# Performance work log

Measured on AMD Instinct MI355X. Metric: run time of the kernel, lower is better.

The kernel has to match this reference:

```python
import jax, jax.numpy as jnp
import numpy as np

NUM_NODES = 50000
NUM_EDGES = 1250000
FEAT_DIM = 64

def setup_inputs() -> dict:
    key = jax.random.key(0)
    k1, k2 = jax.random.split(key)
    msg = jax.random.normal(k1, (NUM_EDGES, FEAT_DIM), dtype=jnp.float32)
    edge_index = jax.random.randint(k2, (2, NUM_EDGES), 0, NUM_NODES, dtype=jnp.int64)
    return {"msg": msg, "edge_index": edge_index}

def reference(msg, edge_index):
    # Original: one_hot(edge_index[1], num_nodes).T @ msg  ==  segment-sum over dst nodes.
    # We compute the same math without materializing the [N, E] one-hot matrix.
    dst = edge_index[1]
    h = jax.ops.segment_sum(msg, dst, num_segments=NUM_NODES)  # [num_nodes, feat_dim]
    return h
```

## Files before the change

kernel.cpp:

```cpp
#include <hip/hip_runtime.h>
#include <hip/hip_bf16.h>

#define NUM_NODES 50000
#define NUM_EDGES 1250000
#define FEAT_DIM  64

#define CAP 80

#define WS_COUNTS   0
#define WS_EDGEIDS  50048

typedef float vfloat4 __attribute__((ext_vector_type(4)));

__global__ void scatter_slots_kernel(const int4* __restrict__ dst4,
                                     int* __restrict__ counts,
                                     int* __restrict__ edge_ids) {
    int t = blockIdx.x * blockDim.x + threadIdx.x;
    if (t < NUM_EDGES / 4) {
        int4 d = dst4[t];
        int e = t * 4;
        int s0 = atomicAdd(&counts[d.x], 1);
        int s1 = atomicAdd(&counts[d.y], 1);
        int s2 = atomicAdd(&counts[d.z], 1);
        int s3 = atomicAdd(&counts[d.w], 1);
        edge_ids[d.x * CAP + s0] = e;
        edge_ids[d.y * CAP + s1] = e + 1;
        edge_ids[d.z * CAP + s2] = e + 2;
        edge_ids[d.w * CAP + s3] = e + 3;
    }
}

__global__ __launch_bounds__(256) void gather_kernel(
    const vfloat4* __restrict__ msg4,
    const int* __restrict__ counts,
    const int* __restrict__ edge_ids,
    vfloat4* __restrict__ out4)
{
    int node  = blockIdx.x * 16 + (threadIdx.x >> 4);
    int chunk = threadIdx.x & 15;
    int cnt = counts[node];
    cnt = (cnt > CAP) ? CAP : cnt;
    const int* ids = edge_ids + node * CAP;
    vfloat4 a0 = 0.f, a1 = 0.f, a2 = 0.f, a3 = 0.f;
    int j = 0;
    for (; j + 3 < cnt; j += 4) {
        int e0 = ids[j];
        int e1 = ids[j + 1];
        int e2 = ids[j + 2];
        int e3 = ids[j + 3];
        a0 += __builtin_nontemporal_load(&msg4[(size_t)e0 * 16 + chunk]);
        a1 += __builtin_nontemporal_load(&msg4[(size_t)e1 * 16 + chunk]);
        a2 += __builtin_nontemporal_load(&msg4[(size_t)e2 * 16 + chunk]);
        a3 += __builtin_nontemporal_load(&msg4[(size_t)e3 * 16 + chunk]);
    }
    for (; j < cnt; j++) {
        int e0 = ids[j];
        a0 += __builtin_nontemporal_load(&msg4[(size_t)e0 * 16 + chunk]);
    }
    out4[(size_t)node * 16 + chunk] = (a0 + a1) + (a2 + a3);
}

extern "C" void kernel_launch(void* const* d_in, const int* in_sizes, int n_in,
                              void* d_out, int out_size, void* d_ws, size_t ws_size,
                              hipStream_t stream) {
    const float* msg = (const float*)d_in[0];
    const int* edge_index = (const int*)d_in[1];
    const int* dst = edge_index + NUM_EDGES;
    float* out = (float*)d_out;

    int* ws       = (int*)d_ws;
    int* counts   = ws + WS_COUNTS;
    int* edge_ids = ws + WS_EDGEIDS;

    hipMemsetAsync(counts, 0, 50048 * sizeof(int), stream);

    scatter_slots_kernel<<<(NUM_EDGES / 4 + 255) / 256, 256, 0, stream>>>(
        (const int4*)dst, counts, edge_ids);

    gather_kernel<<<NUM_NODES / 16, 256, 0, stream>>>(
        (const vfloat4*)msg, counts, edge_ids, (vfloat4*)out);
}
```

Baseline: 495.3 us.

## Assign one wavefront per node with shuffled edge ids and cross-slot reduction

The gather kernel now gives each node a full 64-lane wavefront instead of 16 lanes. Edge ids are loaded cooperatively, one per lane, and broadcast with shuffles. Four slots of 16 lanes each handle a different edge, and the partial sums are combined with xor shuffles before one slot writes the output. This is meant to spread the work better across nodes with varying degree, expose more memory parallelism per node and remove the dependent per-thread id loads. The cost is four times as many blocks, plus shuffle and reduction overhead.

```diff
diff --git a/kernel.cpp b/kernel.cpp
--- a/kernel.cpp
+++ b/kernel.cpp
@@ -36,28 +36,37 @@
     const int* __restrict__ edge_ids,
     vfloat4* __restrict__ out4)
 {
-    int node  = blockIdx.x * 16 + (threadIdx.x >> 4);
-    int chunk = threadIdx.x & 15;
+    int node = blockIdx.x * 4 + (threadIdx.x >> 6);
+    int lane = threadIdx.x & 63;
     int cnt = counts[node];
     cnt = (cnt > CAP) ? CAP : cnt;
     const int* ids = edge_ids + node * CAP;
-    vfloat4 a0 = 0.f, a1 = 0.f, a2 = 0.f, a3 = 0.f;
-    int j = 0;
-    for (; j + 3 < cnt; j += 4) {
-        int e0 = ids[j];
-        int e1 = ids[j + 1];
-        int e2 = ids[j + 2];
-        int e3 = ids[j + 3];
-        a0 += __builtin_nontemporal_load(&msg4[(size_t)e0 * 16 + chunk]);
-        a1 += __builtin_nontemporal_load(&msg4[(size_t)e1 * 16 + chunk]);
-        a2 += __builtin_nontemporal_load(&msg4[(size_t)e2 * 16 + chunk]);
-        a3 += __builtin_nontemporal_load(&msg4[(size_t)e3 * 16 + chunk]);
+    int chunk = lane & 15;
+    int slot  = lane >> 4;
+    vfloat4 acc0 = 0.f, acc1 = 0.f;
+    for (int base = 0; base < cnt; base += 64) {
+        int n = cnt - base;
+        n = (n > 64) ? 64 : n;
+        int eid = (lane < n) ? ids[base + lane] : -1;
+        int T = (n + 3) >> 2;
+        int i = 0;
+        for (; i + 1 < T; i += 2) {
+            int e0 = __shfl(eid, 4 * i + slot);
+            int e1 = __shfl(eid, 4 * i + 4 + slot);
+            if (e0 >= 0) acc0 += __builtin_nontemporal_load(&msg4[(size_t)e0 * 16 + chunk]);
+            if (e1 >= 0) acc1 += __builtin_nontemporal_load(&msg4[(size_t)e1 * 16 + chunk]);
+        }
+        if (i < T) {
+            int e0 = __shfl(eid, 4 * i + slot);
+            if (e0 >= 0) acc0 += __builtin_nontemporal_load(&msg4[(size_t)e0 * 16 + chunk]);
+        }
     }
-    for (; j < cnt; j++) {
-        int e0 = ids[j];
-        a0 += __builtin_nontemporal_load(&msg4[(size_t)e0 * 16 + chunk]);
-    }
-    out4[(size_t)node * 16 + chunk] = (a0 + a1) + (a2 + a3);
+    vfloat4 acc = acc0 + acc1;
+    acc.x += __shfl_xor(acc.x, 16); acc.y += __shfl_xor(acc.y, 16);
+    acc.z += __shfl_xor(acc.z, 16); acc.w += __shfl_xor(acc.w, 16);
+    acc.x += __shfl_xor(acc.x, 32); acc.y += __shfl_xor(acc.y, 32);
+    acc.z += __shfl_xor(acc.z, 32); acc.w += __shfl_xor(acc.w, 32);
+    if (slot == 0) out4[(size_t)node * 16 + chunk] = acc;
 }
 
 extern "C" void kernel_launch(void* const* d_in, const int* in_sizes, int n_in,
@@ -77,6 +86,6 @@
     scatter_slots_kernel<<<(NUM_EDGES / 4 + 255) / 256, 256, 0, stream>>>(
         (const int4*)dst, counts, edge_ids);
 
-    gather_kernel<<<NUM_NODES / 16, 256, 0, stream>>>(
+    gather_kernel<<<NUM_NODES / 4, 256, 0, stream>>>(
         (const vfloat4*)msg, counts, edge_ids, (vfloat4*)out);
 }
```

New measurement: 507.3 us. 2.4% more time.
